# Optimization experiments

Measured on AMD Instinct MI355X. Metric: run time of the kernel, lower is better.

The kernel has to match this reference:

```python
import jax, jax.numpy as jnp
import numpy as np

INPUT_SIZE = 1024
HEAD_SIZE = 64


def setup_inputs() -> dict:
    key = jax.random.key(0)
    kx, kk, kq, kv = jax.random.split(key, 4)
    B, T, C, H = 4, 4096, INPUT_SIZE, HEAD_SIZE
    x = jax.random.normal(kx, (B, T, C), dtype=jnp.float32)
    # nn.Linear(C, H, bias=False) weight is (H, C); we store transposed (C, H)
    # so that y = x @ W matches torch's x @ weight.T
    scale = 1.0 / np.sqrt(C)
    Wk = jax.random.uniform(kk, (C, H), dtype=jnp.float32, minval=-scale, maxval=scale)
    Wq = jax.random.uniform(kq, (C, H), dtype=jnp.float32, minval=-scale, maxval=scale)
    Wv = jax.random.uniform(kv, (C, H), dtype=jnp.float32, minval=-scale, maxval=scale)
    return {"x": x, "Wk": Wk, "Wq": Wq, "Wv": Wv}


def reference(x, Wk, Wq, Wv):
    B, T, C = x.shape
    k = x @ Wk  # (B, T, H)
    q = x @ Wq
    v = x @ Wv
    H = k.shape[-1]
    # scaled scores (B, T, T)
    wei = jnp.einsum('bth,bsh->bts', q, k) * (H ** -0.5)
    causal = jnp.tril(jnp.ones((T, T), dtype=bool))
    wei = jnp.where(causal, wei, -jnp.inf)
    wei = jax.nn.softmax(wei, axis=-1)
    out = jnp.einsum('bts,bsh->bth', wei, v)  # (B, T, H)
    return out
```

## Files before the change

kernel.cpp:

```cpp
#include <hip/hip_runtime.h>
#include <math.h>


#define BT   16384
#define TDIM 4096
#define CDIM 1024
#define HDIM 64
#define ACCW 68
#define NSLOT 288

typedef __attribute__((ext_vector_type(8))) short bf16x8;
typedef __attribute__((ext_vector_type(4))) float f32x4;
typedef __attribute__((ext_vector_type(8))) unsigned short us8;
typedef __attribute__((ext_vector_type(4))) unsigned short us4;

static __device__ __forceinline__ unsigned short f2bf(float f) {
    unsigned int u = __float_as_uint(f);
    u += 0x7fffu + ((u >> 16) & 1u);
    return (unsigned short)(u >> 16);
}

static __device__ __forceinline__ void pswap(unsigned &x, unsigned &y) {
    asm("v_permlane32_swap_b32 %0, %1" : "+v"(x), "+v"(y));
    asm("v_permlane16_swap_b32 %0, %1" : "+v"(x), "+v"(y));
}

static __device__ __forceinline__ void softmax_pack(
    const f32x4 sT[4], bool diag, int qloc, int quad,
    bf16x8 &pa0, bf16x8 &pa1)
{
    float p[4][4];
    if (diag) {
        #pragma unroll
        for (int st = 0; st < 4; st++)
            #pragma unroll
            for (int r = 0; r < 4; r++) {
                int kkloc = st * 16 + quad * 4 + r;
                p[st][r] = (kkloc > qloc) ? 0.f : __expf(sT[st][r]);
            }
    } else {
        #pragma unroll
        for (int st = 0; st < 4; st++)
            #pragma unroll
            for (int r = 0; r < 4; r++)
                p[st][r] = __expf(sT[st][r]);
    }
    unsigned cpk[4][2];
    #pragma unroll
    for (int st = 0; st < 4; st++) {
        asm("v_cvt_pk_bf16_f32 %0, %1, %2"
            : "=v"(cpk[st][0]) : "v"(p[st][0]), "v"(p[st][1]));
        asm("v_cvt_pk_bf16_f32 %0, %1, %2"
            : "=v"(cpk[st][1]) : "v"(p[st][2]), "v"(p[st][3]));
    }
    union { unsigned u[4]; bf16x8 v; } u0, u1;
    unsigned a0 = cpk[0][0], b0 = cpk[1][0]; pswap(a0, b0);
    unsigned a1 = cpk[0][1], b1 = cpk[1][1]; pswap(a1, b1);
    u0.u[0] = a0; u0.u[1] = a1; u0.u[2] = b0; u0.u[3] = b1;
    unsigned a2 = cpk[2][0], b2 = cpk[3][0]; pswap(a2, b2);
    unsigned a3 = cpk[2][1], b3 = cpk[3][1]; pswap(a3, b3);
    u1.u[0] = a2; u1.u[1] = a3; u1.u[2] = b2; u1.u[3] = b3;
    pa0 = u0.v; pa1 = u1.v;
}

__global__ __launch_bounds__(256) void wtrans(
    const float* __restrict__ Wk, const float* __restrict__ Wq,
    const float* __restrict__ Wv, unsigned short* __restrict__ wtg)
{
    int idx = blockIdx.x * 256 + threadIdx.x;
    int mat = idx >> 16;
    int rem = idx & 65535;
    int h = rem >> 10, c = rem & 1023;
    const float* W = (mat == 0) ? Wk : (mat == 1) ? Wq : Wv;
    wtg[idx] = f2bf(W[c * HDIM + h]);
}

__global__ __launch_bounds__(512) void qkv_proj(
    const float* __restrict__ x, const unsigned short* __restrict__ wtg,
    unsigned short* __restrict__ kg, unsigned short* __restrict__ qg,
    unsigned short* __restrict__ vtg)
{
    __shared__ __align__(16) unsigned short xs[2][32][72];
    __shared__ __align__(16) unsigned short wts[2][192][72];
    const int t = threadIdx.x;
    const int lane = t & 63, wv = t >> 6, quad = lane >> 4, l16 = lane & 15;
    const int mt = wv >> 2;
    const int nq = wv & 3;
    const int row0 = blockIdx.x * 32;

    const int xr = t >> 4, xc4 = (t & 15) * 4;
    const int wn = t >> 3, wc8 = (t & 7) * 8;

    f32x4 acc3[3];
    #pragma unroll
    for (int i = 0; i < 3; i++) acc3[i] = (f32x4){0.f, 0.f, 0.f, 0.f};

    const size_t xrow = (size_t)(row0 + xr) * CDIM + xc4;

    float4 xq[8];
    #pragma unroll
    for (int c = 0; c < 8; c++)
        xq[c] = *(const float4*)&x[xrow + c * 64];

    us8 w0 = *(const us8*)&wtg[(size_t)(wn +   0) * CDIM + wc8];
    us8 w1 = *(const us8*)&wtg[(size_t)(wn +  64) * CDIM + wc8];
    us8 w2 = *(const us8*)&wtg[(size_t)(wn + 128) * CDIM + wc8];

    {
        us4 pk = { f2bf(xq[0].x), f2bf(xq[0].y), f2bf(xq[0].z), f2bf(xq[0].w) };
        *(us4*)&xs[0][xr][xc4] = pk;
        *(us8*)&wts[0][wn +   0][wc8] = w0;
        *(us8*)&wts[0][wn +  64][wc8] = w1;
        *(us8*)&wts[0][wn + 128][wc8] = w2;
    }
    xq[0] = *(const float4*)&x[xrow + 8 * 64];
    w0 = *(const us8*)&wtg[(size_t)(wn +   0) * CDIM + 64 + wc8];
    w1 = *(const us8*)&wtg[(size_t)(wn +  64) * CDIM + 64 + wc8];
    w2 = *(const us8*)&wtg[(size_t)(wn + 128) * CDIM + 64 + wc8];
    __syncthreads();

    #pragma unroll
    for (int it = 0; it < 16; it++) {
        const int buf = it & 1;
        if (it + 1 < 16) {
            const int sl = (it + 1) & 7;
            us4 pk = { f2bf(xq[sl].x), f2bf(xq[sl].y),
                       f2bf(xq[sl].z), f2bf(xq[sl].w) };
            *(us4*)&xs[buf ^ 1][xr][xc4] = pk;
            *(us8*)&wts[buf ^ 1][wn +   0][wc8] = w0;
            *(us8*)&wts[buf ^ 1][wn +  64][wc8] = w1;
            *(us8*)&wts[buf ^ 1][wn + 128][wc8] = w2;
            if (it + 9 < 16)
                xq[sl] = *(const float4*)&x[xrow + (it + 9) * 64];
            if (it + 2 < 16) {
                int nc = (it + 2) * 64;
                w0 = *(const us8*)&wtg[(size_t)(wn +   0) * CDIM + nc + wc8];
                w1 = *(const us8*)&wtg[(size_t)(wn +  64) * CDIM + nc + wc8];
                w2 = *(const us8*)&wtg[(size_t)(wn + 128) * CDIM + nc + wc8];
            }
        }
        bf16x8 a0 = *(const bf16x8*)&xs[buf][mt * 16 + l16][quad * 8];
        bf16x8 a1 = *(const bf16x8*)&xs[buf][mt * 16 + l16][32 + quad * 8];
        #pragma unroll
        for (int j = 0; j < 3; j++) {
            int nt = nq * 3 + j;
            bf16x8 b0 = *(const bf16x8*)&wts[buf][nt * 16 + l16][quad * 8];
            bf16x8 b1 = *(const bf16x8*)&wts[buf][nt * 16 + l16][32 + quad * 8];
            acc3[j] = __builtin_amdgcn_mfma_f32_16x16x32_bf16(a0, b0, acc3[j], 0, 0, 0);
            acc3[j] = __builtin_amdgcn_mfma_f32_16x16x32_bf16(a1, b1, acc3[j], 0, 0, 0);
        }
        __syncthreads();
    }

    const int mrow = row0 + mt * 16 + quad * 4;
    #pragma unroll
    for (int j = 0; j < 3; j++) {
        int nt = nq * 3 + j;
        int mat = nt >> 2;
        int col = (nt & 3) * 16 + l16;
        if (mat == 2) {
            int bb = mrow >> 12, tr = mrow & 4095;
            us4 pv = { f2bf(acc3[j][0]), f2bf(acc3[j][1]),
                       f2bf(acc3[j][2]), f2bf(acc3[j][3]) };
            *(us4*)&vtg[((size_t)(bb * HDIM + col) << 12) + tr] = pv;
        } else {
            float s = (mat == 1) ? 0.125f : 1.0f;
            unsigned short* dst = (mat == 0) ? kg : qg;
            #pragma unroll
            for (int reg = 0; reg < 4; reg++)
                dst[(size_t)(mrow + reg) * HDIM + col] = f2bf(acc3[j][reg] * s);
        }
    }
}

__global__ __launch_bounds__(256) void attn(
    const unsigned short* __restrict__ qg, const unsigned short* __restrict__ kg,
    const unsigned short* __restrict__ vtg, float* __restrict__ slabs)
{
    __shared__ __align__(16) unsigned short Ks[2][64][72];
    __shared__ __align__(16) unsigned short Vt[2][64][72];

    const int t = threadIdx.x;
    const int lane = t & 63, wv = t >> 6, quad = lane >> 4, l16 = lane & 15;

    const int b = blockIdx.x / NSLOT;
    const int s = blockIdx.x - b * NSLOT;
    int a;
    if      (s < 8)   a = 0;
    else if (s < 24)  a = 1;
    else if (s < 48)  a = 2;
    else if (s < 80)  a = 3;
    else if (s < 120) a = 4;
    else if (s < 168) a = 5;
    else if (s < 224) a = 6;
    else              a = 7;
    const int u  = s - 4 * a * (a + 1);
    const int qt = a * 8 + u / (a + 1);
    const int c  = u % (a + 1);

    const size_t bbase = (size_t)b * TDIM;
    const int Q0 = qt * 64;
    const int kt0 = c * 8;
    const int kt1 = (kt0 + 7 < qt) ? kt0 + 7 : qt;

    const int qrow = Q0 + wv * 16 + l16;
    const bf16x8 qa0 = *(const bf16x8*)&qg[(bbase + qrow) * HDIM + quad * 8];
    const bf16x8 qa1 = *(const bf16x8*)&qg[(bbase + qrow) * HDIM + 32 + quad * 8];

    const short onev = (l16 == 0) ? (short)0x3F80 : (short)0;
    const bf16x8 ones = { onev, onev, onev, onev, onev, onev, onev, onev };

    f32x4 O[5];
    #pragma unroll
    for (int i = 0; i < 5; i++) O[i] = (f32x4){0.f, 0.f, 0.f, 0.f};

    const int fr = t >> 3, fc = (t & 7) * 8;

    us8 kr0 = *(const us8*)&kg[(bbase + kt0 * 64 + fr) * HDIM + fc];
    us8 kr1 = *(const us8*)&kg[(bbase + kt0 * 64 + fr + 32) * HDIM + fc];
    us8 vr0 = *(const us8*)&vtg[((size_t)(b * HDIM + fr) << 12) + kt0 * 64 + fc];
    us8 vr1 = *(const us8*)&vtg[((size_t)(b * HDIM + fr + 32) << 12) + kt0 * 64 + fc];
    *(us8*)&Ks[0][fr][fc] = kr0;
    *(us8*)&Ks[0][fr + 32][fc] = kr1;
    *(us8*)&Vt[0][fr][fc] = vr0;
    *(us8*)&Vt[0][fr + 32][fc] = vr1;
    if (kt0 < kt1) {
        int kn = kt0 + 1;
        kr0 = *(const us8*)&kg[(bbase + kn * 64 + fr) * HDIM + fc];
        kr1 = *(const us8*)&kg[(bbase + kn * 64 + fr + 32) * HDIM + fc];
        vr0 = *(const us8*)&vtg[((size_t)(b * HDIM + fr) << 12) + kn * 64 + fc];
        vr1 = *(const us8*)&vtg[((size_t)(b * HDIM + fr + 32) << 12) + kn * 64 + fc];
    }
    __syncthreads();

    const int qloc = wv * 16 + l16;

    bf16x8 pa0, pa1;
    {
        f32x4 sT[4];
        #pragma unroll
        for (int st = 0; st < 4; st++) {
            bf16x8 kb0 = *(const bf16x8*)&Ks[0][st * 16 + l16][quad * 8];
            bf16x8 kb1 = *(const bf16x8*)&Ks[0][st * 16 + l16][32 + quad * 8];
            f32x4 z = (f32x4){0.f, 0.f, 0.f, 0.f};
            z = __builtin_amdgcn_mfma_f32_16x16x32_bf16(kb0, qa0, z, 0, 0, 0);
            z = __builtin_amdgcn_mfma_f32_16x16x32_bf16(kb1, qa1, z, 0, 0, 0);
            sT[st] = z;
        }
        softmax_pack(sT, kt0 == qt, qloc, quad, pa0, pa1);
    }

    int buf = 0;
    for (int kt = kt0; kt < kt1; ++kt) {
        *(us8*)&Ks[buf ^ 1][fr][fc] = kr0;
        *(us8*)&Ks[buf ^ 1][fr + 32][fc] = kr1;
        *(us8*)&Vt[buf ^ 1][fr][fc] = vr0;
        *(us8*)&Vt[buf ^ 1][fr + 32][fc] = vr1;
        if (kt + 2 <= kt1) {
            int kn = kt + 2;
            kr0 = *(const us8*)&kg[(bbase + kn * 64 + fr) * HDIM + fc];
            kr1 = *(const us8*)&kg[(bbase + kn * 64 + fr + 32) * HDIM + fc];
            vr0 = *(const us8*)&vtg[((size_t)(b * HDIM + fr) << 12) + kn * 64 + fc];
            vr1 = *(const us8*)&vtg[((size_t)(b * HDIM + fr + 32) << 12) + kn * 64 + fc];
        }
        __syncthreads();

        __builtin_amdgcn_s_setprio(1);
        f32x4 sT[4];
        #pragma unroll
        for (int st = 0; st < 4; st++) {
            bf16x8 kb0 = *(const bf16x8*)&Ks[buf ^ 1][st * 16 + l16][quad * 8];
            bf16x8 kb1 = *(const bf16x8*)&Ks[buf ^ 1][st * 16 + l16][32 + quad * 8];
            f32x4 z = (f32x4){0.f, 0.f, 0.f, 0.f};
            z = __builtin_amdgcn_mfma_f32_16x16x32_bf16(kb0, qa0, z, 0, 0, 0);
            z = __builtin_amdgcn_mfma_f32_16x16x32_bf16(kb1, qa1, z, 0, 0, 0);
            sT[st] = z;
        }
        #pragma unroll
        for (int nt = 0; nt < 4; nt++) {
            bf16x8 vb0 = *(const bf16x8*)&Vt[buf][nt * 16 + l16][quad * 8];
            bf16x8 vb1 = *(const bf16x8*)&Vt[buf][nt * 16 + l16][32 + quad * 8];
            O[nt] = __builtin_amdgcn_mfma_f32_16x16x32_bf16(pa0, vb0, O[nt], 0, 0, 0);
            O[nt] = __builtin_amdgcn_mfma_f32_16x16x32_bf16(pa1, vb1, O[nt], 0, 0, 0);
        }
        O[4] = __builtin_amdgcn_mfma_f32_16x16x32_bf16(pa0, ones, O[4], 0, 0, 0);
        O[4] = __builtin_amdgcn_mfma_f32_16x16x32_bf16(pa1, ones, O[4], 0, 0, 0);
        __builtin_amdgcn_s_setprio(0);

        softmax_pack(sT, (kt + 1) == qt, qloc, quad, pa0, pa1);

        __syncthreads();
        buf ^= 1;
    }

    #pragma unroll
    for (int nt = 0; nt < 4; nt++) {
        bf16x8 vb0 = *(const bf16x8*)&Vt[buf][nt * 16 + l16][quad * 8];
        bf16x8 vb1 = *(const bf16x8*)&Vt[buf][nt * 16 + l16][32 + quad * 8];
        O[nt] = __builtin_amdgcn_mfma_f32_16x16x32_bf16(pa0, vb0, O[nt], 0, 0, 0);
        O[nt] = __builtin_amdgcn_mfma_f32_16x16x32_bf16(pa1, vb1, O[nt], 0, 0, 0);
    }
    O[4] = __builtin_amdgcn_mfma_f32_16x16x32_bf16(pa0, ones, O[4], 0, 0, 0);
    O[4] = __builtin_amdgcn_mfma_f32_16x16x32_bf16(pa1, ones, O[4], 0, 0, 0);

    float* slab = slabs + (size_t)(b * NSLOT + s) * 64 * ACCW;
    const int rl = wv * 16 + quad * 4;
    #pragma unroll
    for (int nt = 0; nt < 4; nt++)
        #pragma unroll
        for (int r = 0; r < 4; r++)
            slab[(size_t)(rl + r) * ACCW + nt * 16 + l16] = O[nt][r];
    if (l16 == 0) {
        #pragma unroll
        for (int r = 0; r < 4; r++)
            slab[(size_t)(rl + r) * ACCW + 64] = O[4][r];
    }
}

__global__ __launch_bounds__(256) void reduce_norm(
    const float* __restrict__ slabs, float* __restrict__ out)
{
    int idx = blockIdx.x * 256 + threadIdx.x;
    int row = idx >> 4, c4 = (idx & 15) * 4;
    int b = row >> 12, qt = (row >> 6) & 63, r64 = row & 63;
    int a = qt >> 3, nc = a + 1;
    int base = 4 * a * (a + 1) + (qt & 7) * nc;

    const float* sl = slabs + ((size_t)(b * NSLOT + base) * 64 + r64) * ACCW;
    float4 o = make_float4(0.f, 0.f, 0.f, 0.f);
    float l = 0.f;
    for (int i = 0; i < nc; i++) {
        float4 v = *(const float4*)&sl[c4];
        o.x += v.x; o.y += v.y; o.z += v.z; o.w += v.w;
        l += sl[64];
        sl += (size_t)64 * ACCW;
    }
    float inv = 1.f / l;
    *(float4*)&out[(size_t)row * HDIM + c4] =
        make_float4(o.x * inv, o.y * inv, o.z * inv, o.w * inv);
}

extern "C" void kernel_launch(void* const* d_in, const int* in_sizes, int n_in,
                              void* d_out, int out_size, void* d_ws, size_t ws_size,
                              hipStream_t stream) {
    const float* x  = (const float*)d_in[0];
    const float* Wk = (const float*)d_in[1];
    const float* Wq = (const float*)d_in[2];
    const float* Wv = (const float*)d_in[3];
    float* out = (float*)d_out;

    unsigned short* wtg = (unsigned short*)d_ws;
    unsigned short* kg  = wtg + 196608;
    unsigned short* qg  = kg + (size_t)BT * HDIM;
    unsigned short* vtg = qg + (size_t)BT * HDIM;
    float* slabs = (float*)(vtg + (size_t)4 * HDIM * TDIM);

    wtrans<<<768, 256, 0, stream>>>(Wk, Wq, Wv, wtg);
    qkv_proj<<<BT / 32, 512, 0, stream>>>(x, wtg, kg, qg, vtg);
    attn<<<4 * NSLOT, 256, 0, stream>>>(qg, kg, vtg, slabs);
    reduce_norm<<<BT * HDIM / (4 * 256), 256, 0, stream>>>(slabs, out);
}
```

Before: 138.3 us.

## Restructure QKV projection into wave-private tiles without block barriers

```diff
diff --git a/kernel.cpp b/kernel.cpp
--- a/kernel.cpp
+++ b/kernel.cpp
@@ -18,6 +18,12 @@
     unsigned int u = __float_as_uint(f);
     u += 0x7fffu + ((u >> 16) & 1u);
     return (unsigned short)(u >> 16);
+}
+
+static __device__ __forceinline__ bf16x8 pack8(float4 lo, float4 hi) {
+    us8 r = { f2bf(lo.x), f2bf(lo.y), f2bf(lo.z), f2bf(lo.w),
+              f2bf(hi.x), f2bf(hi.y), f2bf(hi.z), f2bf(hi.w) };
+    union { us8 u; bf16x8 v; } c; c.u = r; return c.v;
 }
 
 static __device__ __forceinline__ void pswap(unsigned &x, unsigned &y) {
@@ -75,100 +81,102 @@
     wtg[idx] = f2bf(W[c * HDIM + h]);
 }
 
-__global__ __launch_bounds__(512) void qkv_proj(
+__global__ __launch_bounds__(256) void qkv_proj(
     const float* __restrict__ x, const unsigned short* __restrict__ wtg,
     unsigned short* __restrict__ kg, unsigned short* __restrict__ qg,
     unsigned short* __restrict__ vtg)
 {
-    __shared__ __align__(16) unsigned short xs[2][32][72];
-    __shared__ __align__(16) unsigned short wts[2][192][72];
+    __shared__ __align__(16) unsigned short wts[192][72];
     const int t = threadIdx.x;
     const int lane = t & 63, wv = t >> 6, quad = lane >> 4, l16 = lane & 15;
-    const int mt = wv >> 2;
-    const int nq = wv & 3;
     const int row0 = blockIdx.x * 32;
 
-    const int xr = t >> 4, xc4 = (t & 15) * 4;
-    const int wn = t >> 3, wc8 = (t & 7) * 8;
-
-    f32x4 acc3[3];
-    #pragma unroll
-    for (int i = 0; i < 3; i++) acc3[i] = (f32x4){0.f, 0.f, 0.f, 0.f};
-
-    const size_t xrow = (size_t)(row0 + xr) * CDIM + xc4;
-
-    float4 xq[8];
-    #pragma unroll
-    for (int c = 0; c < 8; c++)
-        xq[c] = *(const float4*)&x[xrow + c * 64];
-
-    us8 w0 = *(const us8*)&wtg[(size_t)(wn +   0) * CDIM + wc8];
-    us8 w1 = *(const us8*)&wtg[(size_t)(wn +  64) * CDIM + wc8];
-    us8 w2 = *(const us8*)&wtg[(size_t)(wn + 128) * CDIM + wc8];
-
-    {
-        us4 pk = { f2bf(xq[0].x), f2bf(xq[0].y), f2bf(xq[0].z), f2bf(xq[0].w) };
-        *(us4*)&xs[0][xr][xc4] = pk;
-        *(us8*)&wts[0][wn +   0][wc8] = w0;
-        *(us8*)&wts[0][wn +  64][wc8] = w1;
-        *(us8*)&wts[0][wn + 128][wc8] = w2;
-    }
-    xq[0] = *(const float4*)&x[xrow + 8 * 64];
-    w0 = *(const us8*)&wtg[(size_t)(wn +   0) * CDIM + 64 + wc8];
-    w1 = *(const us8*)&wtg[(size_t)(wn +  64) * CDIM + 64 + wc8];
-    w2 = *(const us8*)&wtg[(size_t)(wn + 128) * CDIM + 64 + wc8];
-    __syncthreads();
+    const int wrb = wv * 48 + (lane >> 3);
+    const int wc8 = (lane & 7) * 8;
+
+    const size_t xr0 = (size_t)(row0 + l16) * CDIM + quad * 8;
+    const size_t xr1 = xr0 + (size_t)16 * CDIM;
+
+    f32x4 acc[2][3];
+    #pragma unroll
+    for (int m = 0; m < 2; m++)
+        #pragma unroll
+        for (int j = 0; j < 3; j++) acc[m][j] = (f32x4){0.f, 0.f, 0.f, 0.f};
+
+    us8 w[6];
+    #pragma unroll
+    for (int d = 0; d < 6; d++)
+        w[d] = *(const us8*)&wtg[(size_t)(wrb + d * 8) * CDIM + wc8];
+    float4 xf[8];
+    #pragma unroll
+    for (int mt = 0; mt < 2; mt++)
+        #pragma unroll
+        for (int kh = 0; kh < 2; kh++) {
+            const size_t base = (mt ? xr1 : xr0) + kh * 32;
+            xf[mt * 4 + kh * 2 + 0] = *(const float4*)&x[base];
+            xf[mt * 4 + kh * 2 + 1] = *(const float4*)&x[base + 4];
+        }
 
     #pragma unroll
     for (int it = 0; it < 16; it++) {
-        const int buf = it & 1;
+        #pragma unroll
+        for (int d = 0; d < 6; d++)
+            *(us8*)&wts[wrb + d * 8][wc8] = w[d];
+
+        bf16x8 a[2][2];
+        #pragma unroll
+        for (int mt = 0; mt < 2; mt++)
+            #pragma unroll
+            for (int kh = 0; kh < 2; kh++)
+                a[mt][kh] = pack8(xf[mt * 4 + kh * 2], xf[mt * 4 + kh * 2 + 1]);
+
         if (it + 1 < 16) {
-            const int sl = (it + 1) & 7;
-            us4 pk = { f2bf(xq[sl].x), f2bf(xq[sl].y),
-                       f2bf(xq[sl].z), f2bf(xq[sl].w) };
-            *(us4*)&xs[buf ^ 1][xr][xc4] = pk;
-            *(us8*)&wts[buf ^ 1][wn +   0][wc8] = w0;
-            *(us8*)&wts[buf ^ 1][wn +  64][wc8] = w1;
-            *(us8*)&wts[buf ^ 1][wn + 128][wc8] = w2;
-            if (it + 9 < 16)
-                xq[sl] = *(const float4*)&x[xrow + (it + 9) * 64];
-            if (it + 2 < 16) {
-                int nc = (it + 2) * 64;
-                w0 = *(const us8*)&wtg[(size_t)(wn +   0) * CDIM + nc + wc8];
-                w1 = *(const us8*)&wtg[(size_t)(wn +  64) * CDIM + nc + wc8];
-                w2 = *(const us8*)&wtg[(size_t)(wn + 128) * CDIM + nc + wc8];
+            const int nc = (it + 1) * 64;
+            #pragma unroll
+            for (int d = 0; d < 6; d++)
+                w[d] = *(const us8*)&wtg[(size_t)(wrb + d * 8) * CDIM + nc + wc8];
+            #pragma unroll
+            for (int mt = 0; mt < 2; mt++)
+                #pragma unroll
+                for (int kh = 0; kh < 2; kh++) {
+                    const size_t base = (mt ? xr1 : xr0) + nc + kh * 32;
+                    xf[mt * 4 + kh * 2 + 0] = *(const float4*)&x[base];
+                    xf[mt * 4 + kh * 2 + 1] = *(const float4*)&x[base + 4];
+                }
+        }
+
+        #pragma unroll
+        for (int j = 0; j < 3; j++) {
+            const int nt = wv * 3 + j;
+            bf16x8 b0 = *(const bf16x8*)&wts[nt * 16 + l16][quad * 8];
+            bf16x8 b1 = *(const bf16x8*)&wts[nt * 16 + l16][32 + quad * 8];
+            acc[0][j] = __builtin_amdgcn_mfma_f32_16x16x32_bf16(a[0][0], b0, acc[0][j], 0, 0, 0);
+            acc[0][j] = __builtin_amdgcn_mfma_f32_16x16x32_bf16(a[0][1], b1, acc[0][j], 0, 0, 0);
+            acc[1][j] = __builtin_amdgcn_mfma_f32_16x16x32_bf16(a[1][0], b0, acc[1][j], 0, 0, 0);
+            acc[1][j] = __builtin_amdgcn_mfma_f32_16x16x32_bf16(a[1][1], b1, acc[1][j], 0, 0, 0);
+        }
+    }
+
+    #pragma unroll
+    for (int mt = 0; mt < 2; mt++) {
+        const int mrow = row0 + mt * 16 + quad * 4;
+        #pragma unroll
+        for (int j = 0; j < 3; j++) {
+            int nt = wv * 3 + j;
+            int mat = nt >> 2;
+            int col = (nt & 3) * 16 + l16;
+            if (mat == 2) {
+                int bb = mrow >> 12, tr = mrow & 4095;
+                us4 pv = { f2bf(acc[mt][j][0]), f2bf(acc[mt][j][1]),
+                           f2bf(acc[mt][j][2]), f2bf(acc[mt][j][3]) };
+                *(us4*)&vtg[((size_t)(bb * HDIM + col) << 12) + tr] = pv;
+            } else {
+                float s = (mat == 1) ? 0.125f : 1.0f;
+                unsigned short* dst = (mat == 0) ? kg : qg;
+                #pragma unroll
+                for (int reg = 0; reg < 4; reg++)
+                    dst[(size_t)(mrow + reg) * HDIM + col] = f2bf(acc[mt][j][reg] * s);
             }
-        }
-        bf16x8 a0 = *(const bf16x8*)&xs[buf][mt * 16 + l16][quad * 8];
-        bf16x8 a1 = *(const bf16x8*)&xs[buf][mt * 16 + l16][32 + quad * 8];
-        #pragma unroll
-        for (int j = 0; j < 3; j++) {
-            int nt = nq * 3 + j;
-            bf16x8 b0 = *(const bf16x8*)&wts[buf][nt * 16 + l16][quad * 8];
-            bf16x8 b1 = *(const bf16x8*)&wts[buf][nt * 16 + l16][32 + quad * 8];
-            acc3[j] = __builtin_amdgcn_mfma_f32_16x16x32_bf16(a0, b0, acc3[j], 0, 0, 0);
-            acc3[j] = __builtin_amdgcn_mfma_f32_16x16x32_bf16(a1, b1, acc3[j], 0, 0, 0);
-        }
-        __syncthreads();
-    }
-
-    const int mrow = row0 + mt * 16 + quad * 4;
-    #pragma unroll
-    for (int j = 0; j < 3; j++) {
-        int nt = nq * 3 + j;
-        int mat = nt >> 2;
-        int col = (nt & 3) * 16 + l16;
-        if (mat == 2) {
-            int bb = mrow >> 12, tr = mrow & 4095;
-            us4 pv = { f2bf(acc3[j][0]), f2bf(acc3[j][1]),
-                       f2bf(acc3[j][2]), f2bf(acc3[j][3]) };
-            *(us4*)&vtg[((size_t)(bb * HDIM + col) << 12) + tr] = pv;
-        } else {
-            float s = (mat == 1) ? 0.125f : 1.0f;
-            unsigned short* dst = (mat == 0) ? kg : qg;
-            #pragma unroll
-            for (int reg = 0; reg < 4; reg++)
-                dst[(size_t)(mrow + reg) * HDIM + col] = f2bf(acc3[j][reg] * s);
         }
     }
 }
@@ -356,7 +364,7 @@
     float* slabs = (float*)(vtg + (size_t)4 * HDIM * TDIM);
 
     wtrans<<<768, 256, 0, stream>>>(Wk, Wq, Wv, wtg);
-    qkv_proj<<<BT / 32, 512, 0, stream>>>(x, wtg, kg, qg, vtg);
+    qkv_proj<<<BT / 32, 256, 0, stream>>>(x, wtg, kg, qg, vtg);
     attn<<<4 * NSLOT, 256, 0, stream>>>(qg, kg, vtg, slabs);
     reduce_norm<<<BT * HDIM / (4 * 256), 256, 0, stream>>>(slabs, out);
 }
```

New measurement: 153.1 us. 10.7% more time.
